# Kernel optimization log

Measured on AMD Instinct MI355X. Metric: run time of the kernel, lower is better.

Reference implementation:

```python
import jax, jax.numpy as jnp
import numpy as np

D_OUT = 256  # out_channels; fourier dim F = D_OUT (Wr has F/2 rows)

def _fourier_pos(H, W, Wr, w1, b1, w2, b2):
    # normalized (H,W) grid in [-1,1], shape [L,2]
    ys = jnp.linspace(-1.0, 1.0, H)
    xs = jnp.linspace(-1.0, 1.0, W)
    gy, gx = jnp.meshgrid(ys, xs, indexing='ij')
    grid = jnp.stack([gy, gx], axis=-1).reshape(-1, 2)  # [L,2]
    proj = grid @ Wr.T                                   # [L,F/2]
    F = 2 * Wr.shape[0]
    feats = jnp.concatenate([jnp.cos(proj), jnp.sin(proj)], axis=-1) / jnp.sqrt(jnp.float32(F))
    h = jax.nn.gelu(feats @ w1.T + b1)
    return h @ w2.T + b2                                 # [L,D_OUT]

def setup_inputs() -> dict:
    key = jax.random.key(0)
    ks = jax.random.split(key, 11)
    N, D, H, W = 16, 256, 128, 128
    s = 1.0 / np.sqrt(D)
    return {
        'x': jax.random.normal(ks[0], (N, D, H, W), jnp.float32),
        'query': jax.random.normal(ks[1], (D_OUT,), jnp.float32),
        'k_w': jax.random.normal(ks[2], (D_OUT, D), jnp.float32) * s,
        'k_b': jax.random.normal(ks[3], (D_OUT,), jnp.float32) * 0.01,
        'v_w': jax.random.normal(ks[4], (D_OUT, D), jnp.float32) * s,
        'v_b': jax.random.normal(ks[5], (D_OUT,), jnp.float32) * 0.01,
        'Wr': jax.random.normal(ks[6], (D_OUT // 2, 2), jnp.float32),
        'w1': jax.random.normal(ks[7], (D_OUT, D_OUT), jnp.float32) * (1.0 / np.sqrt(D_OUT)),
        'b1': jax.random.normal(ks[8], (D_OUT,), jnp.float32) * 0.01,
        'w2': jax.random.normal(ks[9], (D_OUT, D_OUT), jnp.float32) * (1.0 / np.sqrt(D_OUT)),
        'b2': jax.random.normal(ks[10], (D_OUT,), jnp.float32) * 0.01,
    }

def reference(x, query, k_w, k_b, v_w, v_b, Wr, w1, b1, w2, b2):
    N, D, H, W = x.shape
    L = H * W
    tok = x.reshape(N, D, L).transpose(0, 2, 1)          # [N,L,D]
    pos = _fourier_pos(H, W, Wr, w1, b1, w2, b2)         # [L,D_OUT]
    K = tok @ k_w.T + k_b + pos[None]                    # [N,L,D_OUT]
    V = tok @ v_w.T + v_b                                # [N,L,D_OUT]
    scores = jnp.einsum('nld,d->nl', K, query) / jnp.sqrt(jnp.float32(query.shape[0]))
    attn = jax.nn.softmax(scores, axis=1)                # [N,L]
    return jnp.einsum('nl,nld->nd', attn, V)             # [N,D_OUT]
```

## Files before the change

kernel.cpp:

```cpp
#include <hip/hip_runtime.h>
#include <math.h>

#define NB 16
#define DD 256
#define LL 16384
#define DO 256

#define WS_QKP   0
#define WS_QW2P  2048
#define WS_W1T   4096
#define WS_VWT   (WS_W1T + 65536)
#define WS_PQ    (WS_VWT + 65536)
#define WS_M     (WS_PQ + LL)
#define WS_DEN   (WS_M + NB*32)
#define WS_NUM   (WS_DEN + NB*32)

__device__ __forceinline__ float gelu_tanh(float u) {
    float u3 = u*u*u;
    return 0.5f*u*(1.0f + tanhf(0.7978845608028654f*(u + 0.044715f*u3)));
}

__global__ __launch_bounds__(256) void k0(const float* __restrict__ query,
        const float* __restrict__ k_w, const float* __restrict__ w2,
        const float* __restrict__ w1, const float* __restrict__ v_w,
        float* __restrict__ ws) {
    int t = threadIdx.x, b = blockIdx.x;
    if (b < 16) {
        bool is_k = (b < 8);
        int c = b & 7;
        const float* M = is_k ? k_w : w2;
        float a = 0.f;
        #pragma unroll
        for (int oi = 0; oi < 32; ++oi) {
            int o = c*32 + oi;
            a += M[o*DD + t] * query[o];
        }
        ws[(is_k ? WS_QKP : WS_QW2P) + c*256 + t] = a;
    } else if (b < 272) {
        int f = b - 16;
        ws[WS_W1T + f*DO + t] = w1[t*DO + f];
    } else {
        int d = b - 272;
        ws[WS_VWT + d*DO + t] = v_w[t*DD + d];
    }
}

__global__ __launch_bounds__(256) void k1_pq(const float* __restrict__ Wr,
        const float* __restrict__ b1, float* __restrict__ ws) {
    __shared__ __align__(16) float featsT[256*36];
    __shared__ __align__(16) float wbuf[32*256];
    int t = threadIdx.x;
    int w = t >> 6, lane = t & 63;
    int l0 = blockIdx.x * 32;
    int r = t & 127;
    float wr0 = Wr[r*2], wr1 = Wr[r*2+1];
    bool is_cos = (t < 128);
    #pragma unroll 8
    for (int lr = 0; lr < 32; ++lr) {
        int l = l0 + lr;
        int i = l >> 7, j = l & 127;
        float y = -1.0f + (2.0f/127.0f)*(float)i;
        float xg = -1.0f + (2.0f/127.0f)*(float)j;
        float p = y*wr0 + xg*wr1;
        featsT[t*36 + lr] = (is_cos ? cosf(p) : sinf(p)) * 0.0625f;
    }
    int o4 = lane * 4;
    float z[8][4];
    #pragma unroll
    for (int a = 0; a < 8; ++a) { z[a][0]=0.f; z[a][1]=0.f; z[a][2]=0.f; z[a][3]=0.f; }
    float4 qwv; qwv.x = 0.f; qwv.y = 0.f; qwv.z = 0.f; qwv.w = 0.f;
    #pragma unroll
    for (int c = 0; c < 8; ++c) {
        float4 p = *(const float4*)(ws + WS_QW2P + c*256 + o4);
        qwv.x += p.x; qwv.y += p.y; qwv.z += p.z; qwv.w += p.w;
    }
    for (int fc = 0; fc < 8; ++fc) {
        #pragma unroll
        for (int i2 = 0; i2 < 8; ++i2) {
            int idx = i2*256 + t;
            int fl = idx >> 6;
            int c = (idx & 63) * 4;
            *(float4*)(wbuf + fl*256 + c) =
                *(const float4*)(ws + WS_W1T + (fc*32+fl)*DO + c);
        }
        __syncthreads();
        for (int fl = 0; fl < 32; ++fl) {
            float4 wv = *(const float4*)(wbuf + fl*256 + o4);
            const float* fr = featsT + (fc*32+fl)*36 + w*8;
            float4 fa = *(const float4*)(fr);
            float4 fb = *(const float4*)(fr+4);
            float fv[8] = {fa.x,fa.y,fa.z,fa.w,fb.x,fb.y,fb.z,fb.w};
            #pragma unroll
            for (int lr = 0; lr < 8; ++lr) {
                z[lr][0] += fv[lr]*wv.x; z[lr][1] += fv[lr]*wv.y;
                z[lr][2] += fv[lr]*wv.z; z[lr][3] += fv[lr]*wv.w;
            }
        }
        __syncthreads();
    }
    float4 b1v = *(const float4*)(b1 + o4);
    #pragma unroll
    for (int lr = 0; lr < 8; ++lr) {
        float pp = gelu_tanh(z[lr][0]+b1v.x)*qwv.x + gelu_tanh(z[lr][1]+b1v.y)*qwv.y
                 + gelu_tanh(z[lr][2]+b1v.z)*qwv.z + gelu_tanh(z[lr][3]+b1v.w)*qwv.w;
        for (int off = 32; off > 0; off >>= 1) pp += __shfl_xor(pp, off);
        if (lane == 0) ws[WS_PQ + l0 + w*8 + lr] = pp;
    }
}

__global__ __launch_bounds__(256) void k2_main(const float* __restrict__ x,
        float* __restrict__ ws) {
    __shared__ float qk_s[DD];
    __shared__ __align__(16) float e_s[64];
    __shared__ __align__(16) float part[256];
    __shared__ float m_s, den_s, sc_s;
    int t = threadIdx.x;
    int n = blockIdx.x >> 5, lb = blockIdx.x & 31;
    const float* xb = x + (size_t)n * DD * LL + lb * 512;
    int dld = t >> 4, li = (t & 15) * 4;
    int w = t >> 6, lane = t & 63;
    float4 v[2][16];
    #pragma unroll
    for (int i2 = 0; i2 < 16; ++i2)
        v[0][i2] = *(const float4*)(xb + (size_t)(i2*16 + dld)*LL + li);
    float aqk = 0.f;
    #pragma unroll
    for (int c = 0; c < 8; ++c) aqk += ws[WS_QKP + c*256 + t];
    qk_s[t] = aqk;
    if (t == 0) { m_s = -INFINITY; den_s = 0.f; sc_s = 0.f; }
    float pqv[8];
    if (t < 64) {
        #pragma unroll
        for (int tb = 0; tb < 8; ++tb) pqv[tb] = ws[WS_PQ + lb*512 + tb*64 + t];
    }
    __syncthreads();
    float qkr[16];
    #pragma unroll
    for (int i2 = 0; i2 < 16; ++i2) qkr[i2] = qk_s[i2*16 + dld];
    float numacc[16];
    #pragma unroll
    for (int i2 = 0; i2 < 16; ++i2) numacc[i2] = 0.f;
    #pragma unroll
    for (int tb = 0; tb < 8; ++tb) {
        const int cur = tb & 1, nxt = cur ^ 1;
        if (tb < 7) {
            #pragma unroll
            for (int i2 = 0; i2 < 16; ++i2)
                v[nxt][i2] = *(const float4*)(xb + (size_t)(i2*16 + dld)*LL
                                              + (tb+1)*64 + li);
        }
        float sp0=0.f, sp1=0.f, sp2=0.f, sp3=0.f;
        #pragma unroll
        for (int i2 = 0; i2 < 16; ++i2) {
            sp0 += v[cur][i2].x * qkr[i2];
            sp1 += v[cur][i2].y * qkr[i2];
            sp2 += v[cur][i2].z * qkr[i2];
            sp3 += v[cur][i2].w * qkr[i2];
        }
        sp0 += __shfl_xor(sp0, 16); sp0 += __shfl_xor(sp0, 32);
        sp1 += __shfl_xor(sp1, 16); sp1 += __shfl_xor(sp1, 32);
        sp2 += __shfl_xor(sp2, 16); sp2 += __shfl_xor(sp2, 32);
        sp3 += __shfl_xor(sp3, 16); sp3 += __shfl_xor(sp3, 32);
        if (lane < 16) {
            float4 spv; spv.x=sp0; spv.y=sp1; spv.z=sp2; spv.w=sp3;
            *(float4*)(part + w*64 + li) = spv;
        }
        __syncthreads();
        if (t < 64) {
            float dot = part[t] + part[64+t] + part[128+t] + part[192+t];
            float score = (dot + pqv[tb]) * 0.0625f;
            float mc = score;
            for (int off=32; off>0; off>>=1) mc = fmaxf(mc, __shfl_xor(mc, off));
            float mold = m_s;
            float mnew = fmaxf(mold, mc);
            float e = expf(score - mnew);
            e_s[t] = e;
            float dc = e;
            for (int off=32; off>0; off>>=1) dc += __shfl_xor(dc, off);
            if (t == 0) {
                float sc = expf(mold - mnew);
                den_s = den_s*sc + dc;
                m_s = mnew;
                sc_s = sc;
            }
        }
        __syncthreads();
        float sc = sc_s;
        float4 e4 = *(const float4*)(e_s + li);
        #pragma unroll
        for (int i2 = 0; i2 < 16; ++i2) {
            numacc[i2] = numacc[i2]*sc
                + e4.x*v[cur][i2].x + e4.y*v[cur][i2].y
                + e4.z*v[cur][i2].z + e4.w*v[cur][i2].w;
        }
    }
    #pragma unroll
    for (int i2 = 0; i2 < 16; ++i2) {
        float nv = numacc[i2];
        nv += __shfl_xor(nv, 1); nv += __shfl_xor(nv, 2);
        nv += __shfl_xor(nv, 4); nv += __shfl_xor(nv, 8);
        numacc[i2] = nv;
    }
    int pb = n*32 + lb;
    if ((t & 15) == 0) {
        #pragma unroll
        for (int i2 = 0; i2 < 16; ++i2)
            ws[WS_NUM + pb*256 + i2*16 + dld] = numacc[i2];
    }
    if (t == 0) { ws[WS_M + pb] = m_s; ws[WS_DEN + pb] = den_s; }
}

__global__ __launch_bounds__(256) void k3_final(const float* __restrict__ ws,
        const float* __restrict__ v_b, float* __restrict__ out) {
    __shared__ float s_s[DD];
    __shared__ float part[256];
    int t = threadIdx.x;
    int n = blockIdx.x >> 2, oq = blockIdx.x & 3;
    float m = -INFINITY;
    #pragma unroll
    for (int lb = 0; lb < 32; ++lb) m = fmaxf(m, ws[WS_M + n*32 + lb]);
    float den = 0.f, sacc = 0.f;
    #pragma unroll 4
    for (int lb = 0; lb < 32; ++lb) {
        float sc = expf(ws[WS_M + n*32 + lb] - m);
        den += ws[WS_DEN + n*32 + lb] * sc;
        sacc += ws[WS_NUM + (n*32+lb)*256 + t] * sc;
    }
    s_s[t] = sacc / den;
    __syncthreads();
    int w = t >> 6, lane = t & 63;
    int o = oq*64 + lane;
    float acc = 0.f;
    #pragma unroll 8
    for (int i = 0; i < 64; ++i) {
        int d = w*64 + i;
        acc += ws[WS_VWT + d*DO + o] * s_s[d];
    }
    part[t] = acc;
    __syncthreads();
    if (t < 64)
        out[n*DO + oq*64 + t] = v_b[oq*64 + t]
            + part[t] + part[64+t] + part[128+t] + part[192+t];
}

extern "C" void kernel_launch(void* const* d_in, const int* in_sizes, int n_in,
                              void* d_out, int out_size, void* d_ws, size_t ws_size,
                              hipStream_t stream) {
    const float* x     = (const float*)d_in[0];
    const float* query = (const float*)d_in[1];
    const float* k_w   = (const float*)d_in[2];
    const float* v_w   = (const float*)d_in[4];
    const float* v_b   = (const float*)d_in[5];
    const float* Wr    = (const float*)d_in[6];
    const float* w1    = (const float*)d_in[7];
    const float* b1    = (const float*)d_in[8];
    const float* w2    = (const float*)d_in[9];
    float* ws  = (float*)d_ws;
    float* out = (float*)d_out;

    k0<<<528, 256, 0, stream>>>(query, k_w, w2, w1, v_w, ws);
    k1_pq<<<512, 256, 0, stream>>>(Wr, b1, ws);
    k2_main<<<512, 256, 0, stream>>>(x, ws);
    k3_final<<<64, 256, 0, stream>>>(ws, v_b, out);
}
```

Baseline: 450.3 us.

## Fuse positional MLP into main attention kernel and reorganize batch-per-block partials

Merges the positional-projection kernel into the main pass, so each block computes the pq values for its 32 spatial positions in shared memory and then loops over all 16 batches. This removes one kernel launch and the pq round trip through global memory, and the x prefetch is issued before the MLP so the load overlaps that compute. The cost is that every block now writes per-batch partial max, denominator and numerator values (512 partials per batch instead of 32), so the final kernel has to do larger reductions. Barriers use a custom s_waitcnt lgkmcnt plus s_barrier in place of __syncthreads.

```diff
diff --git a/kernel.cpp b/kernel.cpp
--- a/kernel.cpp
+++ b/kernel.cpp
@@ -10,15 +10,20 @@
 #define WS_QW2P  2048
 #define WS_W1T   4096
 #define WS_VWT   (WS_W1T + 65536)
-#define WS_PQ    (WS_VWT + 65536)
-#define WS_M     (WS_PQ + LL)
-#define WS_DEN   (WS_M + NB*32)
-#define WS_NUM   (WS_DEN + NB*32)
+#define WS_M     (WS_VWT + 65536)
+#define WS_DEN   (WS_M + NB*512)
+#define WS_NUM   (WS_DEN + NB*512)
 
 __device__ __forceinline__ float gelu_tanh(float u) {
     float u3 = u*u*u;
     return 0.5f*u*(1.0f + tanhf(0.7978845608028654f*(u + 0.044715f*u3)));
 }
+
+#define LGKMBAR() do {                                          \
+    asm volatile("s_waitcnt lgkmcnt(0)" ::: "memory");          \
+    __builtin_amdgcn_s_barrier();                               \
+    asm volatile("" ::: "memory");                              \
+} while (0)
 
 __global__ __launch_bounds__(256) void k0(const float* __restrict__ query,
         const float* __restrict__ k_w, const float* __restrict__ w2,
@@ -45,190 +50,196 @@
     }
 }
 
-__global__ __launch_bounds__(256) void k1_pq(const float* __restrict__ Wr,
-        const float* __restrict__ b1, float* __restrict__ ws) {
+__global__ __launch_bounds__(256) void k2_fused(const float* __restrict__ x,
+        const float* __restrict__ Wr, const float* __restrict__ b1,
+        float* __restrict__ ws) {
     __shared__ __align__(16) float featsT[256*36];
-    __shared__ __align__(16) float wbuf[32*256];
+    __shared__ float qk_s[DD];
+    __shared__ float pq_s[32];
+    __shared__ __align__(16) float part[128];
+    __shared__ __align__(16) float e_s[32];
     int t = threadIdx.x;
+    int lb = blockIdx.x;
+    int l0 = lb * 32;
     int w = t >> 6, lane = t & 63;
-    int l0 = blockIdx.x * 32;
-    int r = t & 127;
-    float wr0 = Wr[r*2], wr1 = Wr[r*2+1];
-    bool is_cos = (t < 128);
-    #pragma unroll 8
-    for (int lr = 0; lr < 32; ++lr) {
-        int l = l0 + lr;
-        int i = l >> 7, j = l & 127;
-        float y = -1.0f + (2.0f/127.0f)*(float)i;
-        float xg = -1.0f + (2.0f/127.0f)*(float)j;
-        float p = y*wr0 + xg*wr1;
-        featsT[t*36 + lr] = (is_cos ? cosf(p) : sinf(p)) * 0.0625f;
-    }
-    int o4 = lane * 4;
-    float z[8][4];
-    #pragma unroll
-    for (int a = 0; a < 8; ++a) { z[a][0]=0.f; z[a][1]=0.f; z[a][2]=0.f; z[a][3]=0.f; }
-    float4 qwv; qwv.x = 0.f; qwv.y = 0.f; qwv.z = 0.f; qwv.w = 0.f;
-    #pragma unroll
-    for (int c = 0; c < 8; ++c) {
-        float4 p = *(const float4*)(ws + WS_QW2P + c*256 + o4);
-        qwv.x += p.x; qwv.y += p.y; qwv.z += p.z; qwv.w += p.w;
-    }
-    for (int fc = 0; fc < 8; ++fc) {
-        #pragma unroll
-        for (int i2 = 0; i2 < 8; ++i2) {
-            int idx = i2*256 + t;
-            int fl = idx >> 6;
-            int c = (idx & 63) * 4;
-            *(float4*)(wbuf + fl*256 + c) =
-                *(const float4*)(ws + WS_W1T + (fc*32+fl)*DO + c);
-        }
-        __syncthreads();
-        for (int fl = 0; fl < 32; ++fl) {
-            float4 wv = *(const float4*)(wbuf + fl*256 + o4);
-            const float* fr = featsT + (fc*32+fl)*36 + w*8;
-            float4 fa = *(const float4*)(fr);
-            float4 fb = *(const float4*)(fr+4);
-            float fv[8] = {fa.x,fa.y,fa.z,fa.w,fb.x,fb.y,fb.z,fb.w};
-            #pragma unroll
-            for (int lr = 0; lr < 8; ++lr) {
-                z[lr][0] += fv[lr]*wv.x; z[lr][1] += fv[lr]*wv.y;
-                z[lr][2] += fv[lr]*wv.z; z[lr][3] += fv[lr]*wv.w;
-            }
-        }
-        __syncthreads();
-    }
-    float4 b1v = *(const float4*)(b1 + o4);
-    #pragma unroll
-    for (int lr = 0; lr < 8; ++lr) {
-        float pp = gelu_tanh(z[lr][0]+b1v.x)*qwv.x + gelu_tanh(z[lr][1]+b1v.y)*qwv.y
-                 + gelu_tanh(z[lr][2]+b1v.z)*qwv.z + gelu_tanh(z[lr][3]+b1v.w)*qwv.w;
-        for (int off = 32; off > 0; off >>= 1) pp += __shfl_xor(pp, off);
-        if (lane == 0) ws[WS_PQ + l0 + w*8 + lr] = pp;
-    }
-}
-
-__global__ __launch_bounds__(256) void k2_main(const float* __restrict__ x,
-        float* __restrict__ ws) {
-    __shared__ float qk_s[DD];
-    __shared__ __align__(16) float e_s[64];
-    __shared__ __align__(16) float part[256];
-    __shared__ float m_s, den_s, sc_s;
-    int t = threadIdx.x;
-    int n = blockIdx.x >> 5, lb = blockIdx.x & 31;
-    const float* xb = x + (size_t)n * DD * LL + lb * 512;
-    int dld = t >> 4, li = (t & 15) * 4;
-    int w = t >> 6, lane = t & 63;
-    float4 v[2][16];
-    #pragma unroll
-    for (int i2 = 0; i2 < 16; ++i2)
-        v[0][i2] = *(const float4*)(xb + (size_t)(i2*16 + dld)*LL + li);
+    int dld = t >> 3, li4 = (t & 7) * 4;
+    const float* xb = x + l0 + li4;
+
+    float4 vb[2][8];
+    #pragma unroll
+    for (int i2 = 0; i2 < 8; ++i2)
+        vb[0][i2] = *(const float4*)(xb + ((size_t)(0*DD + i2*32 + dld))*LL);
+    #pragma unroll
+    for (int i2 = 0; i2 < 8; ++i2)
+        vb[1][i2] = *(const float4*)(xb + ((size_t)(1*DD + i2*32 + dld))*LL);
+
     float aqk = 0.f;
     #pragma unroll
     for (int c = 0; c < 8; ++c) aqk += ws[WS_QKP + c*256 + t];
     qk_s[t] = aqk;
-    if (t == 0) { m_s = -INFINITY; den_s = 0.f; sc_s = 0.f; }
-    float pqv[8];
-    if (t < 64) {
-        #pragma unroll
-        for (int tb = 0; tb < 8; ++tb) pqv[tb] = ws[WS_PQ + lb*512 + tb*64 + t];
-    }
-    __syncthreads();
-    float qkr[16];
-    #pragma unroll
-    for (int i2 = 0; i2 < 16; ++i2) qkr[i2] = qk_s[i2*16 + dld];
-    float numacc[16];
-    #pragma unroll
-    for (int i2 = 0; i2 < 16; ++i2) numacc[i2] = 0.f;
-    #pragma unroll
-    for (int tb = 0; tb < 8; ++tb) {
-        const int cur = tb & 1, nxt = cur ^ 1;
-        if (tb < 7) {
-            #pragma unroll
-            for (int i2 = 0; i2 < 16; ++i2)
-                v[nxt][i2] = *(const float4*)(xb + (size_t)(i2*16 + dld)*LL
-                                              + (tb+1)*64 + li);
-        }
+
+    {
+        int r = t & 127;
+        float wr0 = Wr[r*2], wr1 = Wr[r*2+1];
+        bool is_cos = (t < 128);
+        #pragma unroll 8
+        for (int lr = 0; lr < 32; ++lr) {
+            int l = l0 + lr;
+            int i = l >> 7, j = l & 127;
+            float y = -1.0f + (2.0f/127.0f)*(float)i;
+            float xg = -1.0f + (2.0f/127.0f)*(float)j;
+            float p = y*wr0 + xg*wr1;
+            featsT[t*36 + lr] = (is_cos ? cosf(p) : sinf(p)) * 0.0625f;
+        }
+    }
+    LGKMBAR();
+
+    float z[8][4];
+    #pragma unroll
+    for (int a = 0; a < 8; ++a) { z[a][0]=0.f; z[a][1]=0.f; z[a][2]=0.f; z[a][3]=0.f; }
+    int o4 = lane * 4;
+    const float* w1p = ws + WS_W1T + o4;
+    const float* frp = featsT + w*8;
+    #pragma unroll 4
+    for (int f = 0; f < 256; ++f) {
+        float4 wv = *(const float4*)(w1p + f*256);
+        float4 fa = *(const float4*)(frp + f*36);
+        float4 fbq = *(const float4*)(frp + f*36 + 4);
+        float fv[8] = {fa.x,fa.y,fa.z,fa.w,fbq.x,fbq.y,fbq.z,fbq.w};
+        #pragma unroll
+        for (int lr = 0; lr < 8; ++lr) {
+            z[lr][0] += fv[lr]*wv.x; z[lr][1] += fv[lr]*wv.y;
+            z[lr][2] += fv[lr]*wv.z; z[lr][3] += fv[lr]*wv.w;
+        }
+    }
+    {
+        float4 qwv; qwv.x=0.f; qwv.y=0.f; qwv.z=0.f; qwv.w=0.f;
+        #pragma unroll
+        for (int c = 0; c < 8; ++c) {
+            float4 p = *(const float4*)(ws + WS_QW2P + c*256 + o4);
+            qwv.x += p.x; qwv.y += p.y; qwv.z += p.z; qwv.w += p.w;
+        }
+        float4 b1v = *(const float4*)(b1 + o4);
+        #pragma unroll
+        for (int lr = 0; lr < 8; ++lr) {
+            float pp = gelu_tanh(z[lr][0]+b1v.x)*qwv.x + gelu_tanh(z[lr][1]+b1v.y)*qwv.y
+                     + gelu_tanh(z[lr][2]+b1v.z)*qwv.z + gelu_tanh(z[lr][3]+b1v.w)*qwv.w;
+            #pragma unroll
+            for (int off = 32; off > 0; off >>= 1) pp += __shfl_xor(pp, off);
+            if (lane == 0) pq_s[w*8 + lr] = pp;
+        }
+    }
+    LGKMBAR();
+
+    float qkr[8];
+    #pragma unroll
+    for (int i2 = 0; i2 < 8; ++i2) qkr[i2] = qk_s[i2*32 + dld];
+
+    #pragma unroll
+    for (int n = 0; n < 16; ++n) {
+        const float4 (&vc)[8] = vb[n & 1];
         float sp0=0.f, sp1=0.f, sp2=0.f, sp3=0.f;
         #pragma unroll
-        for (int i2 = 0; i2 < 16; ++i2) {
-            sp0 += v[cur][i2].x * qkr[i2];
-            sp1 += v[cur][i2].y * qkr[i2];
-            sp2 += v[cur][i2].z * qkr[i2];
-            sp3 += v[cur][i2].w * qkr[i2];
-        }
-        sp0 += __shfl_xor(sp0, 16); sp0 += __shfl_xor(sp0, 32);
-        sp1 += __shfl_xor(sp1, 16); sp1 += __shfl_xor(sp1, 32);
-        sp2 += __shfl_xor(sp2, 16); sp2 += __shfl_xor(sp2, 32);
-        sp3 += __shfl_xor(sp3, 16); sp3 += __shfl_xor(sp3, 32);
-        if (lane < 16) {
-            float4 spv; spv.x=sp0; spv.y=sp1; spv.z=sp2; spv.w=sp3;
-            *(float4*)(part + w*64 + li) = spv;
-        }
-        __syncthreads();
-        if (t < 64) {
-            float dot = part[t] + part[64+t] + part[128+t] + part[192+t];
-            float score = (dot + pqv[tb]) * 0.0625f;
+        for (int i2 = 0; i2 < 8; ++i2) {
+            sp0 += vc[i2].x * qkr[i2];
+            sp1 += vc[i2].y * qkr[i2];
+            sp2 += vc[i2].z * qkr[i2];
+            sp3 += vc[i2].w * qkr[i2];
+        }
+        sp0 += __shfl_xor(sp0, 8); sp0 += __shfl_xor(sp0, 16); sp0 += __shfl_xor(sp0, 32);
+        sp1 += __shfl_xor(sp1, 8); sp1 += __shfl_xor(sp1, 16); sp1 += __shfl_xor(sp1, 32);
+        sp2 += __shfl_xor(sp2, 8); sp2 += __shfl_xor(sp2, 16); sp2 += __shfl_xor(sp2, 32);
+        sp3 += __shfl_xor(sp3, 8); sp3 += __shfl_xor(sp3, 16); sp3 += __shfl_xor(sp3, 32);
+        if (lane < 8) {
+            float4 s4; s4.x=sp0; s4.y=sp1; s4.z=sp2; s4.w=sp3;
+            *(float4*)(part + w*32 + li4) = s4;
+        }
+        LGKMBAR();
+        if (t < 32) {
+            float dot = part[t] + part[32+t] + part[64+t] + part[96+t];
+            float score = (dot + pq_s[t]) * 0.0625f;
             float mc = score;
-            for (int off=32; off>0; off>>=1) mc = fmaxf(mc, __shfl_xor(mc, off));
-            float mold = m_s;
-            float mnew = fmaxf(mold, mc);
-            float e = expf(score - mnew);
+            #pragma unroll
+            for (int off = 16; off > 0; off >>= 1) mc = fmaxf(mc, __shfl_xor(mc, off));
+            float e = expf(score - mc);
             e_s[t] = e;
             float dc = e;
-            for (int off=32; off>0; off>>=1) dc += __shfl_xor(dc, off);
+            #pragma unroll
+            for (int off = 16; off > 0; off >>= 1) dc += __shfl_xor(dc, off);
             if (t == 0) {
-                float sc = expf(mold - mnew);
-                den_s = den_s*sc + dc;
-                m_s = mnew;
-                sc_s = sc;
+                ws[WS_M + n*512 + lb] = mc;
+                ws[WS_DEN + n*512 + lb] = dc;
             }
         }
-        __syncthreads();
-        float sc = sc_s;
-        float4 e4 = *(const float4*)(e_s + li);
-        #pragma unroll
-        for (int i2 = 0; i2 < 16; ++i2) {
-            numacc[i2] = numacc[i2]*sc
-                + e4.x*v[cur][i2].x + e4.y*v[cur][i2].y
-                + e4.z*v[cur][i2].z + e4.w*v[cur][i2].w;
-        }
-    }
-    #pragma unroll
-    for (int i2 = 0; i2 < 16; ++i2) {
-        float nv = numacc[i2];
-        nv += __shfl_xor(nv, 1); nv += __shfl_xor(nv, 2);
-        nv += __shfl_xor(nv, 4); nv += __shfl_xor(nv, 8);
-        numacc[i2] = nv;
-    }
-    int pb = n*32 + lb;
-    if ((t & 15) == 0) {
-        #pragma unroll
-        for (int i2 = 0; i2 < 16; ++i2)
-            ws[WS_NUM + pb*256 + i2*16 + dld] = numacc[i2];
-    }
-    if (t == 0) { ws[WS_M + pb] = m_s; ws[WS_DEN + pb] = den_s; }
+        LGKMBAR();
+        float4 e4 = *(const float4*)(e_s + li4);
+        float na[8];
+        #pragma unroll
+        for (int i2 = 0; i2 < 8; ++i2)
+            na[i2] = e4.x*vc[i2].x + e4.y*vc[i2].y + e4.z*vc[i2].z + e4.w*vc[i2].w;
+        #pragma unroll
+        for (int i2 = 0; i2 < 8; ++i2) {
+            na[i2] += __shfl_xor(na[i2], 1);
+            na[i2] += __shfl_xor(na[i2], 2);
+            na[i2] += __shfl_xor(na[i2], 4);
+        }
+        if ((t & 7) == 0) {
+            #pragma unroll
+            for (int i2 = 0; i2 < 8; ++i2)
+                ws[WS_NUM + ((size_t)n*512 + lb)*256 + i2*32 + dld] = na[i2];
+        }
+        if (n + 2 < 16) {
+            #pragma unroll
+            for (int i2 = 0; i2 < 8; ++i2)
+                vb[n & 1][i2] = *(const float4*)(xb
+                    + ((size_t)((n+2)*DD + i2*32 + dld))*LL);
+        }
+    }
 }
 
 __global__ __launch_bounds__(256) void k3_final(const float* __restrict__ ws,
         const float* __restrict__ v_b, float* __restrict__ out) {
+    __shared__ float red[256];
+    __shared__ float e_sc[512];
     __shared__ float s_s[DD];
-    __shared__ float part[256];
-    int t = threadIdx.x;
-    int n = blockIdx.x >> 2, oq = blockIdx.x & 3;
-    float m = -INFINITY;
-    #pragma unroll
-    for (int lb = 0; lb < 32; ++lb) m = fmaxf(m, ws[WS_M + n*32 + lb]);
-    float den = 0.f, sacc = 0.f;
+    __shared__ __align__(16) float sp[4*256];
+    int t = threadIdx.x, n = blockIdx.x >> 2, oq = blockIdx.x & 3;
+    const float* Mp = ws + WS_M + n*512;
+    const float* Dp = ws + WS_DEN + n*512;
+    float m0 = Mp[t], m1 = Mp[t+256];
+    red[t] = fmaxf(m0, m1);
+    __syncthreads();
+    for (int s = 128; s > 0; s >>= 1) {
+        if (t < s) red[t] = fmaxf(red[t], red[t+s]);
+        __syncthreads();
+    }
+    float m = red[0];
+    __syncthreads();
+    float e0 = expf(m0 - m), e1 = expf(m1 - m);
+    e_sc[t] = e0; e_sc[t+256] = e1;
+    red[t] = Dp[t]*e0 + Dp[t+256]*e1;
+    __syncthreads();
+    for (int s = 128; s > 0; s >>= 1) {
+        if (t < s) red[t] += red[t+s];
+        __syncthreads();
+    }
+    float den = red[0];
+    __syncthreads();
+    int w = t >> 6, lane = t & 63;
+    const float* NBp = ws + WS_NUM + (size_t)n*512*256;
+    float ax=0.f, ay=0.f, az=0.f, aw=0.f;
     #pragma unroll 4
-    for (int lb = 0; lb < 32; ++lb) {
-        float sc = expf(ws[WS_M + n*32 + lb] - m);
-        den += ws[WS_DEN + n*32 + lb] * sc;
-        sacc += ws[WS_NUM + (n*32+lb)*256 + t] * sc;
-    }
-    s_s[t] = sacc / den;
-    __syncthreads();
-    int w = t >> 6, lane = t & 63;
+    for (int i = 0; i < 128; ++i) {
+        int lbq = w*128 + i;
+        float sc = e_sc[lbq];
+        float4 v4 = *(const float4*)(NBp + (size_t)lbq*256 + lane*4);
+        ax += sc*v4.x; ay += sc*v4.y; az += sc*v4.z; aw += sc*v4.w;
+    }
+    { float4 a4; a4.x=ax; a4.y=ay; a4.z=az; a4.w=aw;
+      *(float4*)(sp + w*256 + lane*4) = a4; }
+    __syncthreads();
+    s_s[t] = (sp[t] + sp[256+t] + sp[512+t] + sp[768+t]) / den;
+    __syncthreads();
     int o = oq*64 + lane;
     float acc = 0.f;
     #pragma unroll 8
@@ -236,11 +247,11 @@
         int d = w*64 + i;
         acc += ws[WS_VWT + d*DO + o] * s_s[d];
     }
-    part[t] = acc;
+    red[t] = acc;
     __syncthreads();
     if (t < 64)
         out[n*DO + oq*64 + t] = v_b[oq*64 + t]
-            + part[t] + part[64+t] + part[128+t] + part[192+t];
+            + red[t] + red[64+t] + red[128+t] + red[192+t];
 }
 
 extern "C" void kernel_launch(void* const* d_in, const int* in_sizes, int n_in,
@@ -259,7 +270,6 @@
     float* out = (float*)d_out;
 
     k0<<<528, 256, 0, stream>>>(query, k_w, w2, w1, v_w, ws);
-    k1_pq<<<512, 256, 0, stream>>>(Wr, b1, ws);
-    k2_main<<<512, 256, 0, stream>>>(x, ws);
+    k2_fused<<<512, 256, 0, stream>>>(x, Wr, b1, ws);
     k3_final<<<64, 256, 0, stream>>>(ws, v_b, out);
 }
```

Result: faster. 434.4 us (-3.5%).
